# Optimization experiments

Hardware: AMD Instinct MI355X
Metric: run time of the kernel (lower is better)

The kernel has to match this reference:

```python
import jax, jax.numpy as jnp
import numpy as np

B, H, W, C = 16, 32, 32, 512
NUM_HEADS = 8
ATTN_DIM = 512
HEAD_DIM = ATTN_DIM // NUM_HEADS
EPS = 1e-5


def setup_inputs() -> dict:
    key = jax.random.key(0)
    ks = jax.random.split(key, 6)
    s_in = 1.0 / np.sqrt(C)
    s_attn = 1.0 / np.sqrt(ATTN_DIM)
    return {
        "x": jax.random.normal(ks[0], (B, H, W, C), dtype=jnp.float32),
        "gamma": jnp.ones((C,), dtype=jnp.float32),
        "beta": jnp.zeros((C,), dtype=jnp.float32),
        "wq": jax.random.normal(ks[1], (C, ATTN_DIM), dtype=jnp.float32) * s_in,
        "bq": jnp.zeros((ATTN_DIM,), dtype=jnp.float32),
        "wk": jax.random.normal(ks[2], (C, ATTN_DIM), dtype=jnp.float32) * s_in,
        "bk": jnp.zeros((ATTN_DIM,), dtype=jnp.float32),
        "wv": jax.random.normal(ks[3], (C, ATTN_DIM), dtype=jnp.float32) * s_in,
        "bv": jnp.zeros((ATTN_DIM,), dtype=jnp.float32),
        "wo": jax.random.normal(ks[4], (ATTN_DIM, C), dtype=jnp.float32) * s_attn,
        "bo": jnp.zeros((C,), dtype=jnp.float32),
    }


def reference(x, gamma, beta, wq, bq, wk, bk, wv, bv, wo, bo):
    b, h, w, c = x.shape
    t = h * w  # number of spatial tokens
    # GroupNorm with 1 group: normalize over (H, W, C) per sample
    mean = jnp.mean(x, axis=(1, 2, 3), keepdims=True)
    var = jnp.var(x, axis=(1, 2, 3), keepdims=True)
    xn = (x - mean) * jax.lax.rsqrt(var + EPS) * gamma + beta
    xn = xn.reshape(b, t, c)
    # 1x1-conv q/k/v == dense over channel dim; split into heads
    q = (xn @ wq + bq).reshape(b, t, NUM_HEADS, HEAD_DIM)
    k = (xn @ wk + bk).reshape(b, t, NUM_HEADS, HEAD_DIM)
    v = (xn @ wv + bv).reshape(b, t, NUM_HEADS, HEAD_DIM)
    scale = 1.0 / jnp.sqrt(jnp.asarray(HEAD_DIM, dtype=x.dtype))
    scores = jnp.einsum('bqhd,bkhd->bhqk', q, k) * scale
    probs = jax.nn.softmax(scores, axis=-1)
    attn = jnp.einsum('bhqk,bkhd->bqhd', probs, v).reshape(b, t, ATTN_DIM)
    out = attn @ wo + bo
    # Multiplex([None, branch]): residual add, then Reshape([-1, model_dim])
    return x.reshape(b, t, c) + out
```

## Files before the change

kernel.cpp:

```cpp
#include <hip/hip_runtime.h>
#include <hip/hip_bf16.h>

typedef __attribute__((ext_vector_type(8))) short short8;
typedef __attribute__((ext_vector_type(4))) short short4v;
typedef __attribute__((ext_vector_type(4))) float f32x4;

#define B_ 16
#define T_ 1024
#define C_ 512
#define NH 8
#define HD 64

__device__ __forceinline__ short f2bf(float f) {
  union { float f; unsigned u; } v;
  v.f = f;
  unsigned r = v.u + 0x7fffu + ((v.u >> 16) & 1u);
  return (short)(r >> 16);
}

__device__ __forceinline__ short2 pack_bf2(float a, float b) {
  __hip_bfloat162 t = __float22bfloat162_rn(make_float2(a, b));
  short2 r;
  __builtin_memcpy(&r, &t, 4);
  return r;
}

__device__ __forceinline__ void gload_lds16(const short* g, short* l) {
  __builtin_amdgcn_global_load_lds(
      (const __attribute__((address_space(1))) void*)g,
      (__attribute__((address_space(3))) void*)l, 16, 0, 0);
}

__global__ __launch_bounds__(256) void stats1_kernel(const float* __restrict__ x,
                                                     float2* __restrict__ partials) {
  int chunk = blockIdx.x;
  int b = blockIdx.y;
  int tid = threadIdx.x;
  const float4* xb = (const float4*)(x + (size_t)b * 524288 + (size_t)chunk * 8192);
  float s = 0.f, s2 = 0.f;
#pragma unroll
  for (int i = 0; i < 8; i++) {
    float4 v = xb[tid + i * 256];
    s  += v.x + v.y + v.z + v.w;
    s2 += v.x * v.x + v.y * v.y + v.z * v.z + v.w * v.w;
  }
  __shared__ float ls[256], ls2[256];
  ls[tid] = s; ls2[tid] = s2;
  __syncthreads();
  for (int o = 128; o > 0; o >>= 1) {
    if (tid < o) { ls[tid] += ls[tid + o]; ls2[tid] += ls2[tid + o]; }
    __syncthreads();
  }
  if (tid == 0) partials[b * 64 + chunk] = make_float2(ls[0], ls2[0]);
}

__global__ __launch_bounds__(64) void stats2_kernel(const float2* __restrict__ partials,
                                                    float* __restrict__ stats) {
  int b = blockIdx.x;
  float2 p = partials[b * 64 + threadIdx.x];
  float s = p.x, s2 = p.y;
#pragma unroll
  for (int off = 1; off < 64; off <<= 1) {
    s  += __shfl_xor(s,  off, 64);
    s2 += __shfl_xor(s2, off, 64);
  }
  if (threadIdx.x == 0) {
    float mean = s * (1.f / 524288.f);
    float var  = s2 * (1.f / 524288.f) - mean * mean;
    stats[b * 2]     = mean;
    stats[b * 2 + 1] = rsqrtf(var + 1e-5f);
  }
}

__global__ __launch_bounds__(256) void norm_kernel(const float* __restrict__ x,
                                                   const float* __restrict__ gamma,
                                                   const float* __restrict__ beta,
                                                   const float* __restrict__ stats,
                                                   short* __restrict__ xn) {
  size_t i4 = (size_t)blockIdx.x * 256 + threadIdx.x;
  float4 v = ((const float4*)x)[i4];
  size_t i = i4 * 4;
  int b = (int)(i >> 19);
  int c = (int)(i & 511);
  float mean = stats[b * 2], rstd = stats[b * 2 + 1];
  short4v o;
  o[0] = f2bf((v.x - mean) * rstd * gamma[c + 0] + beta[c + 0]);
  o[1] = f2bf((v.y - mean) * rstd * gamma[c + 1] + beta[c + 1]);
  o[2] = f2bf((v.z - mean) * rstd * gamma[c + 2] + beta[c + 2]);
  o[3] = f2bf((v.w - mean) * rstd * gamma[c + 3] + beta[c + 3]);
  ((short4v*)xn)[i4] = o;
}

__global__ __launch_bounds__(256) void transpose_w_all(const float* __restrict__ wq,
                                                       const float* __restrict__ wk,
                                                       const float* __restrict__ wv,
                                                       const float* __restrict__ wo,
                                                       short* __restrict__ wqkvT,
                                                       short* __restrict__ woT) {
  int o = blockIdx.x * 256 + threadIdx.x;
  int sel = o >> 18;
  int oo = o & 262143;
  int k = oo >> 9, n = oo & 511;
  const float* w = (sel == 0) ? wq : (sel == 1) ? wk : (sel == 2) ? wv : wo;
  float val = w[oo];
  if (sel < 3) wqkvT[((size_t)(sel * 512 + n)) * 512 + k] = f2bf(val);
  else         woT[(size_t)n * 512 + k] = f2bf(val);
}

__global__ __launch_bounds__(256) void gemm_qkv(const short* __restrict__ A,
                                                const short* __restrict__ Bt,
                                                const float* __restrict__ bq,
                                                const float* __restrict__ bk,
                                                const float* __restrict__ bv,
                                                short* __restrict__ C) {
  __shared__ __align__(16) short As[128 * 32];
  __shared__ __align__(16) short Bs[128 * 32];
  int tid = threadIdx.x;
  int w = tid >> 6, lane = tid & 63;
  int quad = lane >> 4, l16 = lane & 15;
  int mw = (w >> 1) * 64, nw = (w & 1) * 64;
  int seg = (blockIdx.x * 128) >> 9;
  const float* bias = (seg == 0) ? bq : (seg == 1) ? bk : bv;
  float smul = (seg == 0) ? 0.125f : 1.0f;
  const short* Atile = A + (size_t)(blockIdx.y * 128) * 512;
  const short* Btile = Bt + (size_t)(blockIdx.x * 128) * 512;
  int srow = (w << 4) + (lane >> 2);
  int scol = (lane & 3) * 8;
  f32x4 acc[4][4] = {};
  for (int k0 = 0; k0 < 512; k0 += 32) {
    __syncthreads();
    gload_lds16(&Atile[(size_t)srow * 512 + k0 + scol],        &As[w * 512]);
    gload_lds16(&Atile[(size_t)(srow + 64) * 512 + k0 + scol], &As[2048 + w * 512]);
    gload_lds16(&Btile[(size_t)srow * 512 + k0 + scol],        &Bs[w * 512]);
    gload_lds16(&Btile[(size_t)(srow + 64) * 512 + k0 + scol], &Bs[2048 + w * 512]);
    __syncthreads();
    short8 af[4], bf[4];
#pragma unroll
    for (int i = 0; i < 4; i++) af[i] = *(const short8*)(&As[(mw + i * 16 + l16) * 32 + quad * 8]);
#pragma unroll
    for (int i = 0; i < 4; i++) bf[i] = *(const short8*)(&Bs[(nw + i * 16 + l16) * 32 + quad * 8]);
#pragma unroll
    for (int mi = 0; mi < 4; mi++)
#pragma unroll
      for (int ni = 0; ni < 4; ni++)
        acc[mi][ni] = __builtin_amdgcn_mfma_f32_16x16x32_bf16(af[mi], bf[ni], acc[mi][ni], 0, 0, 0);
  }
  int m0 = blockIdx.y * 128 + mw;
  int n0 = blockIdx.x * 128 + nw;
#pragma unroll
  for (int mi = 0; mi < 4; mi++)
#pragma unroll
    for (int ni = 0; ni < 4; ni++) {
      int col = n0 + ni * 16 + l16;
      float bval = bias[col & 511];
#pragma unroll
      for (int r = 0; r < 4; r++) {
        int row = m0 + mi * 16 + quad * 4 + r;
        C[(size_t)row * 1536 + col] = f2bf((acc[mi][ni][r] + bval) * smul);
      }
    }
}

__global__ __launch_bounds__(256) void gemm_out(const short* __restrict__ A,
                                                const short* __restrict__ Bt,
                                                const float* __restrict__ bias,
                                                const float* __restrict__ xres,
                                                float* __restrict__ out) {
  __shared__ __align__(16) short As[128 * 32];
  __shared__ __align__(16) short Bs[128 * 32];
  int tid = threadIdx.x;
  int w = tid >> 6, lane = tid & 63;
  int quad = lane >> 4, l16 = lane & 15;
  int mw = (w >> 1) * 64, nw = (w & 1) * 64;
  const short* Atile = A + (size_t)(blockIdx.y * 128) * 512;
  const short* Btile = Bt + (size_t)(blockIdx.x * 128) * 512;
  int srow = (w << 4) + (lane >> 2);
  int scol = (lane & 3) * 8;
  f32x4 acc[4][4] = {};
  for (int k0 = 0; k0 < 512; k0 += 32) {
    __syncthreads();
    gload_lds16(&Atile[(size_t)srow * 512 + k0 + scol],        &As[w * 512]);
    gload_lds16(&Atile[(size_t)(srow + 64) * 512 + k0 + scol], &As[2048 + w * 512]);
    gload_lds16(&Btile[(size_t)srow * 512 + k0 + scol],        &Bs[w * 512]);
    gload_lds16(&Btile[(size_t)(srow + 64) * 512 + k0 + scol], &Bs[2048 + w * 512]);
    __syncthreads();
    short8 af[4], bf[4];
#pragma unroll
    for (int i = 0; i < 4; i++) af[i] = *(const short8*)(&As[(mw + i * 16 + l16) * 32 + quad * 8]);
#pragma unroll
    for (int i = 0; i < 4; i++) bf[i] = *(const short8*)(&Bs[(nw + i * 16 + l16) * 32 + quad * 8]);
#pragma unroll
    for (int mi = 0; mi < 4; mi++)
#pragma unroll
      for (int ni = 0; ni < 4; ni++)
        acc[mi][ni] = __builtin_amdgcn_mfma_f32_16x16x32_bf16(af[mi], bf[ni], acc[mi][ni], 0, 0, 0);
  }
  int m0 = blockIdx.y * 128 + mw;
  int n0 = blockIdx.x * 128 + nw;
#pragma unroll
  for (int mi = 0; mi < 4; mi++)
#pragma unroll
    for (int ni = 0; ni < 4; ni++) {
      int col = n0 + ni * 16 + l16;
      float bval = bias[col];
#pragma unroll
      for (int r = 0; r < 4; r++) {
        int row = m0 + mi * 16 + quad * 4 + r;
        out[(size_t)row * 512 + col] = acc[mi][ni][r] + bval + xres[(size_t)row * 512 + col];
      }
    }
}

__global__ __launch_bounds__(256) void vtrans_kernel(const short* __restrict__ qkv,
                                                     short* __restrict__ vT) {
  int tt = blockIdx.x;
  int h  = blockIdx.y;
  int b  = blockIdx.z;
  int tid = threadIdx.x;
  __shared__ short TB[64 * 72];
  const short* src = qkv + ((size_t)b * T_) * 1536 + 1024 + (size_t)h * 64;
#pragma unroll
  for (int i = 0; i < 2; i++) {
    int idx = tid + i * 256;
    int t = idx >> 3, c = idx & 7;
    short8 vv = *(const short8*)(src + (size_t)(tt * 64 + t) * 1536 + c * 8);
    *(short8*)(&TB[t * 72 + c * 8]) = vv;
  }
  __syncthreads();
  short* dst = vT + (((size_t)b * NH + h) * HD) * T_ + tt * 64;
#pragma unroll
  for (int i = 0; i < 2; i++) {
    int idx = tid + i * 256;
    int d = idx >> 3, c = idx & 7;
    short8 o;
#pragma unroll
    for (int j = 0; j < 8; j++) o[j] = TB[(c * 8 + j) * 72 + d];
    *(short8*)(dst + (size_t)d * T_ + c * 8) = o;
  }
}

__global__ __launch_bounds__(256) void attn_kernel(const short* __restrict__ Q,
                                                   const short* __restrict__ Kmat,
                                                   const short* __restrict__ vT,
                                                   short* __restrict__ O) {
  int tid = threadIdx.x;
  int w = tid >> 6, lane = tid & 63;
  int quad = lane >> 4, l16 = lane & 15;
  int bh = blockIdx.x;
  int qt = blockIdx.y;
  int b = bh >> 3, h = bh & 7;
  size_t base  = ((size_t)b * T_) * 1536 + (size_t)h * 64;
  size_t vbase = (((size_t)b * NH + h) * HD) * T_;
  size_t obase = ((size_t)b * T_) * 512 + (size_t)h * 64;
  int qrow = qt * 64 + w * 16;

  short8 qf0 = *(const short8*)(Q + base + (size_t)(qrow + l16) * 1536 + quad * 8);
  short8 qf1 = *(const short8*)(Q + base + (size_t)(qrow + l16) * 1536 + quad * 8 + 32);

  __shared__ __align__(16) short KT[64 * 72];
  __shared__ __align__(16) short VT[64 * 72];
  __shared__ __align__(16) short PL[4][16 * 72];

  f32x4 of[4] = {};
  float lsum = 0.f;

  for (int kk0 = 0; kk0 < T_; kk0 += 64) {
    __syncthreads();
#pragma unroll
    for (int i = 0; i < 2; i++) {
      int idx = tid + i * 256;
      int r0 = idx >> 3, c = idx & 7;
      short8 kv = *(const short8*)(Kmat + base + (size_t)(kk0 + r0) * 1536 + c * 8);
      *(short8*)(&KT[r0 * 72 + c * 8]) = kv;
      short8 vv = *(const short8*)(vT + vbase + (size_t)r0 * T_ + kk0 + c * 8);
      *(short8*)(&VT[r0 * 72 + c * 8]) = vv;
    }
    __syncthreads();

#pragma unroll
    for (int t = 0; t < 4; t++) {
      short8 kf0 = *(const short8*)(&KT[(t * 16 + l16) * 72 + quad * 8]);
      short8 kf1 = *(const short8*)(&KT[(t * 16 + l16) * 72 + quad * 8 + 32]);
      f32x4 z = {};
      z = __builtin_amdgcn_mfma_f32_16x16x32_bf16(kf0, qf0, z, 0, 0, 0);
      z = __builtin_amdgcn_mfma_f32_16x16x32_bf16(kf1, qf1, z, 0, 0, 0);
      float p0 = __expf(z[0]), p1 = __expf(z[1]);
      float p2 = __expf(z[2]), p3 = __expf(z[3]);
      lsum += (p0 + p1) + (p2 + p3);
      short2 lo = pack_bf2(p0, p1), hi = pack_bf2(p2, p3);
      short4v pk; pk[0] = lo.x; pk[1] = lo.y; pk[2] = hi.x; pk[3] = hi.y;
      *(short4v*)(&PL[w][l16 * 72 + t * 16 + quad * 4]) = pk;
    }

#pragma unroll
    for (int kc = 0; kc < 2; kc++) {
      short8 pf = *(const short8*)(&PL[w][l16 * 72 + kc * 32 + quad * 8]);
#pragma unroll
      for (int f = 0; f < 4; f++) {
        short8 vf = *(const short8*)(&VT[(f * 16 + l16) * 72 + kc * 32 + quad * 8]);
        of[f] = __builtin_amdgcn_mfma_f32_16x16x32_bf16(pf, vf, of[f], 0, 0, 0);
      }
    }
  }

  lsum += __shfl_xor(lsum, 16, 64);
  lsum += __shfl_xor(lsum, 32, 64);

#pragma unroll
  for (int r = 0; r < 4; r++) {
    float lv = __shfl(lsum, quad * 4 + r, 64);
    float linv = __frcp_rn(lv);
    int row = qrow + quad * 4 + r;
#pragma unroll
    for (int f = 0; f < 4; f++)
      O[obase + (size_t)row * 512 + f * 16 + l16] = f2bf(of[f][r] * linv);
  }
}

extern "C" void kernel_launch(void* const* d_in, const int* in_sizes, int n_in,
                              void* d_out, int out_size, void* d_ws, size_t ws_size,
                              hipStream_t stream) {
  const float* x     = (const float*)d_in[0];
  const float* gamma = (const float*)d_in[1];
  const float* beta  = (const float*)d_in[2];
  const float* wq    = (const float*)d_in[3];
  const float* bq    = (const float*)d_in[4];
  const float* wk    = (const float*)d_in[5];
  const float* bk    = (const float*)d_in[6];
  const float* wv    = (const float*)d_in[7];
  const float* bv    = (const float*)d_in[8];
  const float* wo    = (const float*)d_in[9];
  const float* bo    = (const float*)d_in[10];
  float* out = (float*)d_out;

  char* ws = (char*)d_ws;
  const size_t XN_ELEMS = (size_t)B_ * T_ * C_;
  size_t off = 0;
  float* stats = (float*)(ws + off); off += 256;
  float2* partials = (float2*)(ws + off); off += 16 * 64 * sizeof(float2);
  short* xn    = (short*)(ws + off); off += XN_ELEMS * 2;
  short* wqkvT = (short*)(ws + off); off += (size_t)1536 * 512 * 2;
  short* woT   = (short*)(ws + off); off += (size_t)512 * 512 * 2;
  short* qkv   = (short*)(ws + off); off += (size_t)B_ * T_ * 1536 * 2;
  short* vTb   = (short*)(ws + off); off += XN_ELEMS * 2;
  short* ao    = (short*)(ws + off); off += XN_ELEMS * 2;

  stats1_kernel<<<dim3(64, 16), 256, 0, stream>>>(x, partials);
  stats2_kernel<<<16, 64, 0, stream>>>(partials, stats);
  norm_kernel<<<8192, 256, 0, stream>>>(x, gamma, beta, stats, xn);
  transpose_w_all<<<4096, 256, 0, stream>>>(wq, wk, wv, wo, wqkvT, woT);

  gemm_qkv<<<dim3(12, 128), 256, 0, stream>>>(xn, wqkvT, bq, bk, bv, qkv);

  vtrans_kernel<<<dim3(16, 8, 16), 256, 0, stream>>>(qkv, vTb);
  attn_kernel<<<dim3(128, 16), 256, 0, stream>>>(qkv, qkv + 512, vTb, ao);

  gemm_out<<<dim3(4, 128), 256, 0, stream>>>(ao, woT, bo, x, out);
}
```

Before: 264.8 us.

## Split attention keys across waves with register-resident P and cross-wave reduction

Instead of each wave owning 16 query rows and sharing K/V tiles through LDS, each wave now owns all 64 query rows of the block and a disjoint slice of keys, loading K and V fragments straight from global memory into registers. The softmax probabilities are packed directly into MFMA operands in registers, which removes the per-tile LDS staging and the two barriers per iteration. Partial outputs and denominators are reduced across the four waves through LDS at the end, and the output is written with vectorized stores. In exchange the kernel holds more accumulator registers, issues uncached-style global loads per wave with no LDS reuse of K/V, and serializes the final reduction across waves.

Result: slower. 282.2 us (+6.6%).

```diff
diff --git a/kernel.cpp b/kernel.cpp
--- a/kernel.cpp
+++ b/kernel.cpp
@@ -252,69 +252,101 @@
   size_t base  = ((size_t)b * T_) * 1536 + (size_t)h * 64;
   size_t vbase = (((size_t)b * NH + h) * HD) * T_;
   size_t obase = ((size_t)b * T_) * 512 + (size_t)h * 64;
-  int qrow = qt * 64 + w * 16;
-
-  short8 qf0 = *(const short8*)(Q + base + (size_t)(qrow + l16) * 1536 + quad * 8);
-  short8 qf1 = *(const short8*)(Q + base + (size_t)(qrow + l16) * 1536 + quad * 8 + 32);
-
-  __shared__ __align__(16) short KT[64 * 72];
-  __shared__ __align__(16) short VT[64 * 72];
-  __shared__ __align__(16) short PL[4][16 * 72];
-
-  f32x4 of[4] = {};
-  float lsum = 0.f;
-
-  for (int kk0 = 0; kk0 < T_; kk0 += 64) {
-    __syncthreads();
-#pragma unroll
-    for (int i = 0; i < 2; i++) {
-      int idx = tid + i * 256;
-      int r0 = idx >> 3, c = idx & 7;
-      short8 kv = *(const short8*)(Kmat + base + (size_t)(kk0 + r0) * 1536 + c * 8);
-      *(short8*)(&KT[r0 * 72 + c * 8]) = kv;
-      short8 vv = *(const short8*)(vT + vbase + (size_t)r0 * T_ + kk0 + c * 8);
-      *(short8*)(&VT[r0 * 72 + c * 8]) = vv;
-    }
-    __syncthreads();
-
-#pragma unroll
-    for (int t = 0; t < 4; t++) {
-      short8 kf0 = *(const short8*)(&KT[(t * 16 + l16) * 72 + quad * 8]);
-      short8 kf1 = *(const short8*)(&KT[(t * 16 + l16) * 72 + quad * 8 + 32]);
-      f32x4 z = {};
-      z = __builtin_amdgcn_mfma_f32_16x16x32_bf16(kf0, qf0, z, 0, 0, 0);
-      z = __builtin_amdgcn_mfma_f32_16x16x32_bf16(kf1, qf1, z, 0, 0, 0);
-      float p0 = __expf(z[0]), p1 = __expf(z[1]);
-      float p2 = __expf(z[2]), p3 = __expf(z[3]);
-      lsum += (p0 + p1) + (p2 + p3);
-      short2 lo = pack_bf2(p0, p1), hi = pack_bf2(p2, p3);
-      short4v pk; pk[0] = lo.x; pk[1] = lo.y; pk[2] = hi.x; pk[3] = hi.y;
-      *(short4v*)(&PL[w][l16 * 72 + t * 16 + quad * 4]) = pk;
-    }
-
-#pragma unroll
-    for (int kc = 0; kc < 2; kc++) {
-      short8 pf = *(const short8*)(&PL[w][l16 * 72 + kc * 32 + quad * 8]);
-#pragma unroll
-      for (int f = 0; f < 4; f++) {
-        short8 vf = *(const short8*)(&VT[(f * 16 + l16) * 72 + kc * 32 + quad * 8]);
-        of[f] = __builtin_amdgcn_mfma_f32_16x16x32_bf16(pf, vf, of[f], 0, 0, 0);
-      }
-    }
-  }
-
-  lsum += __shfl_xor(lsum, 16, 64);
-  lsum += __shfl_xor(lsum, 32, 64);
-
-#pragma unroll
-  for (int r = 0; r < 4; r++) {
-    float lv = __shfl(lsum, quad * 4 + r, 64);
-    float linv = __frcp_rn(lv);
-    int row = qrow + quad * 4 + r;
-#pragma unroll
-    for (int f = 0; f < 4; f++)
-      O[obase + (size_t)row * 512 + f * 16 + l16] = f2bf(of[f][r] * linv);
-  }
+  int qrow0 = qt * 64;
+
+  short8 qf0[4], qf1[4];
+#pragma unroll
+  for (int g = 0; g < 4; g++) {
+    const short* qp = Q + base + (size_t)(qrow0 + g * 16 + l16) * 1536 + quad * 8;
+    qf0[g] = *(const short8*)qp;
+    qf1[g] = *(const short8*)(qp + 32);
+  }
+
+  f32x4 oacc[4][4] = {};
+  float lsum[4] = {0.f, 0.f, 0.f, 0.f};
+
+  for (int kk0 = 0; kk0 < T_; kk0 += 128) {
+    int ka = kk0 + w * 16;
+    int kb = ka + 64;
+    const short* kpa = Kmat + base + (size_t)(ka + l16) * 1536 + quad * 8;
+    const short* kpb = Kmat + base + (size_t)(kb + l16) * 1536 + quad * 8;
+    short8 kfa0 = *(const short8*)kpa;
+    short8 kfa1 = *(const short8*)(kpa + 32);
+    short8 kfb0 = *(const short8*)kpb;
+    short8 kfb1 = *(const short8*)(kpb + 32);
+    short8 vf[4];
+#pragma unroll
+    for (int f = 0; f < 4; f++) {
+      const short* vp = vT + vbase + (size_t)(f * 16 + l16) * 1024 + quad * 4;
+      short4v va = *(const short4v*)(vp + ka);
+      short4v vb = *(const short4v*)(vp + kb);
+      short8 t;
+      t[0] = va[0]; t[1] = va[1]; t[2] = va[2]; t[3] = va[3];
+      t[4] = vb[0]; t[5] = vb[1]; t[6] = vb[2]; t[7] = vb[3];
+      vf[f] = t;
+    }
+#pragma unroll
+    for (int g = 0; g < 4; g++) {
+      f32x4 za = {}, zb = {};
+      za = __builtin_amdgcn_mfma_f32_16x16x32_bf16(kfa0, qf0[g], za, 0, 0, 0);
+      za = __builtin_amdgcn_mfma_f32_16x16x32_bf16(kfa1, qf1[g], za, 0, 0, 0);
+      zb = __builtin_amdgcn_mfma_f32_16x16x32_bf16(kfb0, qf0[g], zb, 0, 0, 0);
+      zb = __builtin_amdgcn_mfma_f32_16x16x32_bf16(kfb1, qf1[g], zb, 0, 0, 0);
+      float pa0 = __expf(za[0]), pa1 = __expf(za[1]);
+      float pa2 = __expf(za[2]), pa3 = __expf(za[3]);
+      float pb0 = __expf(zb[0]), pb1 = __expf(zb[1]);
+      float pb2 = __expf(zb[2]), pb3 = __expf(zb[3]);
+      lsum[g] += (pa0 + pa1) + (pa2 + pa3) + (pb0 + pb1) + (pb2 + pb3);
+      short2 a01 = pack_bf2(pa0, pa1), a23 = pack_bf2(pa2, pa3);
+      short2 b01 = pack_bf2(pb0, pb1), b23 = pack_bf2(pb2, pb3);
+      short8 pf;
+      pf[0] = a01.x; pf[1] = a01.y; pf[2] = a23.x; pf[3] = a23.y;
+      pf[4] = b01.x; pf[5] = b01.y; pf[6] = b23.x; pf[7] = b23.y;
+#pragma unroll
+      for (int f = 0; f < 4; f++)
+        oacc[f][g] = __builtin_amdgcn_mfma_f32_16x16x32_bf16(vf[f], pf, oacc[f][g], 0, 0, 0);
+    }
+  }
+
+#pragma unroll
+  for (int g = 0; g < 4; g++) {
+    lsum[g] += __shfl_xor(lsum[g], 16, 64);
+    lsum[g] += __shfl_xor(lsum[g], 32, 64);
+  }
+
+  __shared__ __align__(16) float Lbuf[64 * 68];
+  __shared__ float denomL[4 * 64];
+  if (quad == 0) {
+#pragma unroll
+    for (int g = 0; g < 4; g++) denomL[w * 64 + g * 16 + l16] = lsum[g];
+  }
+  for (int ww = 0; ww < 4; ww++) {
+    __syncthreads();
+    if (w == ww) {
+#pragma unroll
+      for (int g = 0; g < 4; g++)
+#pragma unroll
+        for (int f = 0; f < 4; f++) {
+          float* p = &Lbuf[(g * 16 + l16) * 68 + f * 16 + quad * 4];
+          if (ww == 0) *(f32x4*)p = oacc[f][g];
+          else         *(f32x4*)p = *(f32x4*)p + oacc[f][g];
+        }
+    }
+  }
+  __syncthreads();
+
+  int q = tid >> 2, seg = tid & 3;
+  float dn = denomL[q] + denomL[64 + q] + denomL[128 + q] + denomL[192 + q];
+  float rinv = __frcp_rn(dn);
+  const float* row = &Lbuf[q * 68 + seg * 16];
+  short8 o0, o1;
+#pragma unroll
+  for (int i = 0; i < 8; i++) o0[i] = f2bf(row[i] * rinv);
+#pragma unroll
+  for (int i = 0; i < 8; i++) o1[i] = f2bf(row[8 + i] * rinv);
+  short* op = O + obase + (size_t)(qrow0 + q) * 512 + seg * 16;
+  *(short8*)op = o0;
+  *(short8*)(op + 8) = o1;
 }
 
 extern "C" void kernel_launch(void* const* d_in, const int* in_sizes, int n_in,
```
